# Kernel tuning notes

Hardware: AMD Instinct MI355X
Metric: run time of the kernel (lower is better)

## Reference

```python
import jax, jax.numpy as jnp
import numpy as np

B, CIN, T = 16, 80, 2048
C = 768          # channels
M = 512          # n_embeddings
D = 64           # z_dim
H = 256          # c_dim
N_MLP = 4        # hidden Linear(C, C) layers
LN_EPS = 1e-5
COMMIT = 0.25


def setup_inputs() -> dict:
    key = jax.random.key(0)
    ks = jax.random.split(key, 12)
    s = 0.02
    mels = jax.random.normal(ks[0], (B, CIN, T), dtype=jnp.float32)
    conv_w = jax.random.normal(ks[1], (C, CIN, 4), dtype=jnp.float32) * s  # [out, in, k]
    ln_gamma = jnp.ones((N_MLP + 1, C), dtype=jnp.float32)
    ln_beta = jnp.zeros((N_MLP + 1, C), dtype=jnp.float32)
    w_hidden = jax.random.normal(ks[2], (N_MLP, C, C), dtype=jnp.float32) * s  # [i, out, in]
    w_out = jax.random.normal(ks[3], (D, C), dtype=jnp.float32) * s
    embedding = jax.random.uniform(ks[4], (M, D), dtype=jnp.float32,
                                   minval=-1.0 / 512, maxval=1.0 / 512)
    w_ih = jax.random.normal(ks[5], (4 * H, D), dtype=jnp.float32) * s
    w_hh = jax.random.normal(ks[6], (4 * H, H), dtype=jnp.float32) * s
    b_ih = jnp.zeros((4 * H,), dtype=jnp.float32)
    b_hh = jnp.zeros((4 * H,), dtype=jnp.float32)
    return {"mels": mels, "conv_w": conv_w, "ln_gamma": ln_gamma, "ln_beta": ln_beta,
            "w_hidden": w_hidden, "w_out": w_out, "embedding": embedding,
            "w_ih": w_ih, "w_hh": w_hh, "b_ih": b_ih, "b_hh": b_hh}


def _layer_norm(x, g, b):
    mu = jnp.mean(x, axis=-1, keepdims=True)
    var = jnp.mean(jnp.square(x - mu), axis=-1, keepdims=True)
    return (x - mu) * jax.lax.rsqrt(var + LN_EPS) * g + b


def _lstm(x, w_ih, w_hh, b_ih, b_hh):
    # x: [B, T, D] -> outputs [B, T, H]; torch gate order i, f, g, o
    xg = jnp.einsum('btd,gd->btg', x, w_ih) + b_ih + b_hh  # precompute input gates

    def step(carry, xg_t):
        h, c = carry
        gates = xg_t + h @ w_hh.T
        i, f, g, o = jnp.split(gates, 4, axis=-1)
        c = jax.nn.sigmoid(f) * c + jax.nn.sigmoid(i) * jnp.tanh(g)
        h = jax.nn.sigmoid(o) * jnp.tanh(c)
        return (h, c), h

    h0 = jnp.zeros((x.shape[0], H), dtype=x.dtype)
    (_, _), hs = jax.lax.scan(step, (h0, h0), jnp.swapaxes(xg, 0, 1))
    return jnp.swapaxes(hs, 0, 1)


def reference(mels, conv_w, ln_gamma, ln_beta, w_hidden, w_out, embedding,
              w_ih, w_hh, b_ih, b_hh):
    # Conv1d(k=4, stride=2, pad=1, no bias): [B, CIN, T] -> [B, C, T//2]
    h = jax.lax.conv_general_dilated(
        mels, conv_w, window_strides=(2,), padding=[(1, 1)],
        dimension_numbers=('NCH', 'OIH', 'NCH'))
    h = jnp.swapaxes(h, 1, 2)  # [B, T', C]

    for i in range(N_MLP):
        h = jax.nn.relu(_layer_norm(h, ln_gamma[i], ln_beta[i]))
        h = h @ w_hidden[i].T
    h = jax.nn.relu(_layer_norm(h, ln_gamma[N_MLP], ln_beta[N_MLP]))
    z_beforeVQ = h @ w_out.T  # [B, T', D]

    # VQEmbeddingEMA forward (eval mode: no EMA buffer updates)
    x = z_beforeVQ
    x_flat = jax.lax.stop_gradient(x).reshape(-1, D)  # [N, D]
    dist = (jnp.sum(embedding ** 2, axis=1)[None, :]
            + jnp.sum(x_flat ** 2, axis=1, keepdims=True)
            - 2.0 * x_flat @ embedding.T)  # [N, M]
    indices = jnp.argmin(dist, axis=-1)
    quantized = embedding[indices].reshape(x.shape)
    loss = COMMIT * jnp.mean(jnp.square(x - jax.lax.stop_gradient(quantized)))
    quantized_st = x + jax.lax.stop_gradient(quantized - x)
    counts = jax.ops.segment_sum(jnp.ones_like(indices, dtype=jnp.float32),
                                 indices, num_segments=M)
    avg_probs = counts / x_flat.shape[0]
    perplexity = jnp.exp(-jnp.sum(avg_probs * jnp.log(avg_probs + 1e-10)))

    c = _lstm(quantized_st, w_ih, w_hh, b_ih, b_hh)  # [B, T', H]
    return quantized_st, c, z_beforeVQ, loss, perplexity
```

## Files before the change

kernel.cpp:

```cpp
#include <hip/hip_runtime.h>
#include <hip/hip_bf16.h>
#include <cstdint>

typedef _Float16 half2v __attribute__((ext_vector_type(2)));
typedef short bf16x8 __attribute__((ext_vector_type(8)));
typedef float f32x4v __attribute__((ext_vector_type(4)));

#define DI __device__ __forceinline__

DI half2v bch(float f)    { return __builtin_bit_cast(half2v, f); }
DI half2v bcu(unsigned u) { return __builtin_bit_cast(half2v, u); }

DI float fdot2f(half2v a, half2v b, float c) {
#if __has_builtin(__builtin_amdgcn_fdot2)
  return __builtin_amdgcn_fdot2(a, b, c, false);
#else
  return c + (float)a[0] * (float)b[0] + (float)a[1] * (float)b[1];
#endif
}

DI unsigned short bf16rne(float f) {
  unsigned u = __float_as_uint(f);
  unsigned r = (u + 0x7fffu + ((u >> 16) & 1u)) >> 16;
  return (unsigned short)r;
}
DI float bf16tof(unsigned short h) { return __uint_as_float(((unsigned)h) << 16); }

DI float blockReduceSum(float v, float* sbuf) {
  for (int off = 32; off; off >>= 1) v += __shfl_xor(v, off, 64);
  int wid = threadIdx.x >> 6;
  if ((threadIdx.x & 63) == 0) sbuf[wid] = v;
  __syncthreads();
  float r = sbuf[0] + sbuf[1] + sbuf[2] + sbuf[3];
  __syncthreads();
  return r;
}

__global__ __launch_bounds__(256) void prep_kernel(
    const float* __restrict__ conv_w, const float* __restrict__ w_hh,
    const float* __restrict__ w_ih, const float* __restrict__ b_ih,
    const float* __restrict__ b_hh, const float* __restrict__ emb,
    float* __restrict__ wT, _Float16* __restrict__ whhh,
    float* __restrict__ wihT, float* __restrict__ bias2,
    float* __restrict__ esq, int* __restrict__ counts)
{
  int idx = blockIdx.x * 256 + threadIdx.x;
  if (idx < 245760) {
    int c = idx % 768, rest = idx / 768;
    wT[idx] = conv_w[c * 320 + rest];
  }
  int i1 = idx - 245760;
  if (i1 >= 0 && i1 < 262144) whhh[i1] = (_Float16)w_hh[i1];
  int i2 = idx - (245760 + 262144);
  if (i2 >= 0 && i2 < 65536) {
    int d = i2 >> 10, grow = i2 & 1023;
    wihT[i2] = w_ih[grow * 64 + d];
  }
  int i3 = idx - (245760 + 262144 + 65536);
  if (i3 >= 0 && i3 < 1024) bias2[i3] = b_ih[i3] + b_hh[i3];
  int i4 = idx - (245760 + 262144 + 65536 + 1024);
  if (i4 >= 0 && i4 < 512) {
    float s = 0.f;
    for (int d = 0; d < 64; ++d) { float v = emb[i4 * 64 + d]; s += v * v; }
    esq[i4] = s;
  }
  int i5 = idx - (245760 + 262144 + 65536 + 1024 + 512);
  if (i5 >= 0 && i5 < 512) counts[i5] = 0;
}

__global__ __launch_bounds__(256) void wsplit_kernel(
    const float* __restrict__ w, unsigned short* __restrict__ whi,
    unsigned short* __restrict__ wlo)
{
  int idx = blockIdx.x * 256 + threadIdx.x;
  float v = w[idx];
  unsigned short h = bf16rne(v);
  whi[idx] = h;
  wlo[idx] = bf16rne(v - bf16tof(h));
}

__global__ __launch_bounds__(256) void conv_kernel(
    const float* __restrict__ mels, const float* __restrict__ wT,
    float* __restrict__ out)
{
  __shared__ float xs[80][68];
  const int bx = blockIdx.x;
  const int cblk = bx % 6;
  const int rb = bx / 6;
  const int b = rb >> 5;
  const int t0 = (rb & 31) << 5;
  const int tid = threadIdx.x;
  const int g0 = 2 * t0 - 1;
  for (int e = tid; e < 80 * 68; e += 256) {
    int ci = e / 68, ix = e % 68;
    int g = g0 + ix;
    float v = 0.f;
    if (ix < 67 && g >= 0 && g < 2048) v = mels[((size_t)b * 80 + ci) * 2048 + g];
    xs[ci][ix] = v;
  }
  __syncthreads();
  const int tc = tid & 31, tt = tid >> 5;
  const int c = cblk * 128 + tc * 4;
  float acc[4][4] = {};
  for (int ci = 0; ci < 80; ++ci) {
    float m[10];
#pragma unroll
    for (int r = 0; r < 10; ++r) m[r] = xs[ci][tt * 8 + r];
#pragma unroll
    for (int k = 0; k < 4; ++k) {
      float4 wv = *(const float4*)&wT[(size_t)(ci * 4 + k) * 768 + c];
#pragma unroll
      for (int i = 0; i < 4; ++i) {
        float mv = m[2 * i + k];
        acc[i][0] += mv * wv.x; acc[i][1] += mv * wv.y;
        acc[i][2] += mv * wv.z; acc[i][3] += mv * wv.w;
      }
    }
  }
#pragma unroll
  for (int i = 0; i < 4; ++i) {
    int tp = t0 + tt * 4 + i;
    float4 v = make_float4(acc[i][0], acc[i][1], acc[i][2], acc[i][3]);
    *(float4*)&out[((size_t)b * 1024 + tp) * 768 + c] = v;
  }
}

template<int MODE>
__global__ __launch_bounds__(256) void ln_relu_kernel(
    const float* __restrict__ in, float* __restrict__ outf,
    unsigned short* __restrict__ ohi, unsigned short* __restrict__ olo,
    const float* __restrict__ gamma, const float* __restrict__ beta)
{
  __shared__ float sbuf[4];
  const int row = blockIdx.x, tid = threadIdx.x;
  const float* p = in + (size_t)row * 768;
  float v0 = p[tid], v1 = p[tid + 256], v2 = p[tid + 512];
  float s = blockReduceSum(v0 + v1 + v2, sbuf);
  float mean = s * (1.f / 768.f);
  float d0 = v0 - mean, d1 = v1 - mean, d2 = v2 - mean;
  float sq = blockReduceSum(d0 * d0 + d1 * d1 + d2 * d2, sbuf);
  float rstd = rsqrtf(sq * (1.f / 768.f) + 1e-5f);
  float y0 = fmaxf(d0 * rstd * gamma[tid]       + beta[tid],       0.f);
  float y1 = fmaxf(d1 * rstd * gamma[tid + 256] + beta[tid + 256], 0.f);
  float y2 = fmaxf(d2 * rstd * gamma[tid + 512] + beta[tid + 512], 0.f);
  if (MODE == 0) {
    float* q = outf + (size_t)row * 768;
    q[tid] = y0; q[tid + 256] = y1; q[tid + 512] = y2;
  } else {
    unsigned short* qh = ohi + (size_t)row * 768;
    unsigned short* ql = olo + (size_t)row * 768;
    unsigned short h0 = bf16rne(y0), h1 = bf16rne(y1), h2 = bf16rne(y2);
    qh[tid] = h0; qh[tid + 256] = h1; qh[tid + 512] = h2;
    ql[tid]       = bf16rne(y0 - bf16tof(h0));
    ql[tid + 256] = bf16rne(y1 - bf16tof(h1));
    ql[tid + 512] = bf16rne(y2 - bf16tof(h2));
  }
}

__global__ __launch_bounds__(256) void mlp_gemm(
    const unsigned short* __restrict__ Ahi, const unsigned short* __restrict__ Alo,
    const unsigned short* __restrict__ Whi, const unsigned short* __restrict__ Wlo,
    float* __restrict__ C)
{
  __shared__ unsigned short As[128][40];
  __shared__ unsigned short Bs[128][40];
  const int tid = threadIdx.x;
  const int lane = tid & 63, wid = tid >> 6;
  const int wm = wid >> 1, wn = wid & 1;
  const int l15 = lane & 15, kg = lane >> 4;
  const size_t row0 = (size_t)blockIdx.y * 128;
  const int col0 = blockIdx.x * 128;
  f32x4v acc[4][4];
#pragma unroll
  for (int i = 0; i < 4; ++i)
#pragma unroll
    for (int j = 0; j < 4; ++j) acc[i][j] = (f32x4v){0.f, 0.f, 0.f, 0.f};
  for (int s = 0; s < 3; ++s) {
    const unsigned short* Ap = (s == 2) ? Alo : Ahi;
    const unsigned short* Wp = (s == 1) ? Wlo : Whi;
    for (int kt = 0; kt < 768; kt += 32) {
      __syncthreads();
#pragma unroll
      for (int it = 0; it < 2; ++it) {
        int sidx = tid + it * 256;
        int r = sidx >> 2, kc = (sidx & 3) << 3;
        uint4 va = *(const uint4*)&Ap[(row0 + r) * 768 + kt + kc];
        *(uint4*)&As[r][kc] = va;
        uint4 vb = *(const uint4*)&Wp[(size_t)(col0 + r) * 768 + kt + kc];
        *(uint4*)&Bs[r][kc] = vb;
      }
      __syncthreads();
      bf16x8 af[4], bfr[4];
#pragma unroll
      for (int mf = 0; mf < 4; ++mf)
        af[mf] = *(const bf16x8*)&As[wm * 64 + mf * 16 + l15][kg * 8];
#pragma unroll
      for (int nf = 0; nf < 4; ++nf)
        bfr[nf] = *(const bf16x8*)&Bs[wn * 64 + nf * 16 + l15][kg * 8];
#pragma unroll
      for (int mf = 0; mf < 4; ++mf)
#pragma unroll
        for (int nf = 0; nf < 4; ++nf)
          acc[mf][nf] = __builtin_amdgcn_mfma_f32_16x16x32_bf16(
              af[mf], bfr[nf], acc[mf][nf], 0, 0, 0);
    }
  }
#pragma unroll
  for (int mf = 0; mf < 4; ++mf)
#pragma unroll
    for (int nf = 0; nf < 4; ++nf)
#pragma unroll
      for (int r = 0; r < 4; ++r)
        C[(row0 + wm * 64 + mf * 16 + kg * 4 + r) * 768 +
          col0 + wn * 64 + nf * 16 + l15] = acc[mf][nf][r];
}

template<int BM, int BN, int BK, int TM, int TN>
__global__ __launch_bounds__(256) void gemm_nt(
    const float* __restrict__ A, const float* __restrict__ B,
    float* __restrict__ C, int M, int N, int K)
{
  constexpr int LDA = BM + 4, LDB = BN + 4;
  __shared__ float As[BK][LDA];
  __shared__ float Bs[BK][LDB];
  const int tid = threadIdx.x;
  const size_t row0 = (size_t)blockIdx.y * BM;
  const size_t col0 = (size_t)blockIdx.x * BN;
  const int tx = tid & 15, ty = tid >> 4;
  constexpr int GSM = BM * 4 / TM;
  constexpr int GSN = BN * 4 / TN;
  constexpr int F4R = BK / 4;
  constexpr int AIT = BM * BK / 4 / 256;
  constexpr int BIT = BN * BK / 4 / 256;
  static_assert(AIT * 256 * 4 == BM * BK, "A tile divisibility");
  static_assert(BIT * 256 * 4 == BN * BK, "B tile divisibility");
  float acc[TM][TN] = {};
  for (int kt = 0; kt < K; kt += BK) {
#pragma unroll
    for (int p = 0; p < AIT; ++p) {
      int item = tid + p * 256;
      int r = item / F4R, q = item % F4R;
      float4 v = *(const float4*)&A[(row0 + r) * K + kt + q * 4];
      As[q * 4 + 0][r] = v.x; As[q * 4 + 1][r] = v.y;
      As[q * 4 + 2][r] = v.z; As[q * 4 + 3][r] = v.w;
    }
#pragma unroll
    for (int p = 0; p < BIT; ++p) {
      int item = tid + p * 256;
      int r = item / F4R, q = item % F4R;
      float4 v = *(const float4*)&B[(col0 + r) * K + kt + q * 4];
      Bs[q * 4 + 0][r] = v.x; Bs[q * 4 + 1][r] = v.y;
      Bs[q * 4 + 2][r] = v.z; Bs[q * 4 + 3][r] = v.w;
    }
    __syncthreads();
#pragma unroll
    for (int k = 0; k < BK; ++k) {
      float a[TM], b[TN];
#pragma unroll
      for (int g = 0; g < TM / 4; ++g) {
        float4 v = *(const float4*)&As[k][ty * 4 + g * GSM];
        a[g * 4 + 0] = v.x; a[g * 4 + 1] = v.y; a[g * 4 + 2] = v.z; a[g * 4 + 3] = v.w;
      }
#pragma unroll
      for (int g = 0; g < TN / 4; ++g) {
        float4 v = *(const float4*)&Bs[k][tx * 4 + g * GSN];
        b[g * 4 + 0] = v.x; b[g * 4 + 1] = v.y; b[g * 4 + 2] = v.z; b[g * 4 + 3] = v.w;
      }
#pragma unroll
      for (int i = 0; i < TM; ++i)
#pragma unroll
        for (int j = 0; j < TN; ++j)
          acc[i][j] += a[i] * b[j];
    }
    __syncthreads();
  }
#pragma unroll
  for (int i = 0; i < TM; ++i) {
    size_t row = row0 + ty * 4 + (i >> 2) * GSM + (i & 3);
#pragma unroll
    for (int g = 0; g < TN / 4; ++g) {
      float4 v = make_float4(acc[i][g * 4 + 0], acc[i][g * 4 + 1],
                             acc[i][g * 4 + 2], acc[i][g * 4 + 3]);
      *(float4*)&C[row * N + col0 + tx * 4 + g * GSN] = v;
    }
  }
}

DI unsigned int ordbits(float f) {
  unsigned int u = __float_as_uint(f);
  return (u & 0x80000000u) ? ~u : (u | 0x80000000u);
}

__global__ __launch_bounds__(128) void vq_argmin_kernel(
    const float* __restrict__ dots, const float* __restrict__ esq,
    const float* __restrict__ emb, const float* __restrict__ z,
    float* __restrict__ quant, int* __restrict__ counts,
    float* __restrict__ lossrow)
{
  __shared__ unsigned long long sred[2];
  const int row = blockIdx.x, tid = threadIdx.x;
  float4 d4 = *(const float4*)&dots[(size_t)row * 512 + tid * 4];
  float4 e4 = *(const float4*)&esq[tid * 4];
  float dist[4] = { e4.x - 2.f * d4.x, e4.y - 2.f * d4.y,
                    e4.z - 2.f * d4.z, e4.w - 2.f * d4.w };
  unsigned long long best =
      ((unsigned long long)ordbits(dist[0]) << 32) | (unsigned)(tid * 4);
#pragma unroll
  for (int c2 = 1; c2 < 4; ++c2) {
    unsigned long long k =
        ((unsigned long long)ordbits(dist[c2]) << 32) | (unsigned)(tid * 4 + c2);
    best = (k < best) ? k : best;
  }
  for (int off = 32; off; off >>= 1) {
    unsigned long long o = __shfl_xor(best, off, 64);
    best = (o < best) ? o : best;
  }
  if ((tid & 63) == 0) sred[tid >> 6] = best;
  __syncthreads();
  unsigned long long fin = sred[0] < sred[1] ? sred[0] : sred[1];
  int bi = (int)(fin & 0xffffffffu);
  if (tid < 64) {
    float e = emb[(size_t)bi * 64 + tid];
    quant[(size_t)row * 64 + tid] = e;
    float df = z[(size_t)row * 64 + tid] - e;
    float s = df * df;
    for (int off = 32; off; off >>= 1) s += __shfl_xor(s, off, 64);
    if (tid == 0) {
      lossrow[row] = s;
      atomicAdd(&counts[bi], 1);
    }
  }
}

__global__ __launch_bounds__(256) void finalize_kernel(
    const float* __restrict__ lossrow, const int* __restrict__ counts,
    float* __restrict__ loss_out, float* __restrict__ perp_out)
{
  __shared__ float sbuf[4];
  const int tid = threadIdx.x;
  float s = 0.f;
  for (int i = tid; i < 16384; i += 256) s += lossrow[i];
  s = blockReduceSum(s, sbuf);
  float t = 0.f;
  for (int e = tid; e < 512; e += 256) {
    float p = (float)counts[e] * (1.f / 16384.f);
    t += p * logf(p + 1e-10f);
  }
  t = blockReduceSum(t, sbuf);
  if (tid == 0) {
    *loss_out = 0.25f * s / (16384.f * 64.f);
    *perp_out = expf(-t);
  }
}

__global__ __launch_bounds__(256) void xg_kernel(
    const float* __restrict__ q, const float* __restrict__ wihT,
    const float* __restrict__ bias2, float* __restrict__ xg3)
{
  __shared__ float qs[8][64];
  const int r0 = blockIdx.x * 8, tid = threadIdx.x;
  for (int e = tid; e < 512; e += 256)
    qs[e >> 6][e & 63] = q[(size_t)r0 * 64 + e];
  __syncthreads();
  float4 bias = *(const float4*)&bias2[tid * 4];
  float4 acc[8];
#pragma unroll
  for (int r = 0; r < 8; ++r) acc[r] = bias;
  for (int d = 0; d < 64; ++d) {
    float4 wv = *(const float4*)&wihT[d * 1024 + tid * 4];
#pragma unroll
    for (int r = 0; r < 8; ++r) {
      float qv = qs[r][d];
      acc[r].x += qv * wv.x; acc[r].y += qv * wv.y;
      acc[r].z += qv * wv.z; acc[r].w += qv * wv.w;
    }
  }
#pragma unroll
  for (int r = 0; r < 8; ++r)
    *(float4*)&xg3[(size_t)(r0 + r) * 1024 + tid * 4] = acc[r];
}

#define W24(M) M(0) M(1) M(2) M(3) M(4) M(5) M(6) M(7) M(8) M(9) M(10) M(11) \
               M(12) M(13) M(14) M(15) M(16) M(17) M(18) M(19) M(20) M(21) M(22) M(23)
#define DECLW(J) uint4 wa##J = pA[J]; uint4 wb##J = pB[J];
#define DOTR(J) { float4 h4 = hb4[J]; \
  a0 = fdot2f(bcu(wa##J.x), bch(h4.x), a0); b0 = fdot2f(bcu(wb##J.x), bch(h4.x), b0); \
  a1 = fdot2f(bcu(wa##J.y), bch(h4.y), a1); b1 = fdot2f(bcu(wb##J.y), bch(h4.y), b1); \
  a0 = fdot2f(bcu(wa##J.z), bch(h4.z), a0); b0 = fdot2f(bcu(wb##J.z), bch(h4.z), b0); \
  a1 = fdot2f(bcu(wa##J.w), bch(h4.w), a1); b1 = fdot2f(bcu(wb##J.w), bch(h4.w), b1); }

__global__
__attribute__((amdgpu_flat_work_group_size(512, 512), amdgpu_waves_per_eu(2, 2)))
void lstm_kernel(
    const float* __restrict__ xg3, const _Float16* __restrict__ whhh,
    float* __restrict__ cout)
{
  __shared__ unsigned wlds[1024 * 36];
  __shared__ __align__(16) _Float16 hb[256];
  __shared__ float gbuf[512];
  const int tid = threadIdx.x;
  const int b = blockIdx.x;
  const int jloc = tid & 255;
  const int half = tid >> 8;
  const int rA = half * 256 + jloc;
  const int rB = 512 + half * 256 + jloc;
  {
    const unsigned* wsrc = (const unsigned*)whhh;
    for (int idx = tid; idx < 1024 * 32; idx += 512) {
      int row = idx >> 5, kp = idx & 31;
      wlds[row * 36 + kp] = wsrc[row * 128 + 96 + kp];
    }
  }
  if (tid < 256) hb[tid] = (_Float16)0.f;
  const uint4* pA = (const uint4*)(whhh + (size_t)rA * 256);
  const uint4* pB = (const uint4*)(whhh + (size_t)rB * 256);
  W24(DECLW)
  const size_t bT = (size_t)b * 1024;
  const int rA36 = rA * 36, rB36 = rB * 36;
  float cst = 0.f;
  float xgA = xg3[bT * 1024 + rA];
  float xgB = xg3[bT * 1024 + rB];
  __syncthreads();
  for (int t = 0; t < 1024; ++t) {
    float nxA = 0.f, nxB = 0.f;
    if (t < 1023) {
      nxA = xg3[(bT + t + 1) * 1024 + rA];
      nxB = xg3[(bT + t + 1) * 1024 + rB];
    }
    float a0 = 0.f, a1 = 0.f, b0 = 0.f, b1 = 0.f;
    const float4* hb4 = (const float4*)hb;
    W24(DOTR)
#pragma unroll
    for (int j = 0; j < 8; ++j) {
      float4 h4 = hb4[24 + j];
      uint4 wa = *(const uint4*)&wlds[rA36 + 4 * j];
      uint4 wb = *(const uint4*)&wlds[rB36 + 4 * j];
      a0 = fdot2f(bcu(wa.x), bch(h4.x), a0); b0 = fdot2f(bcu(wb.x), bch(h4.x), b0);
      a1 = fdot2f(bcu(wa.y), bch(h4.y), a1); b1 = fdot2f(bcu(wb.y), bch(h4.y), b1);
      a0 = fdot2f(bcu(wa.z), bch(h4.z), a0); b0 = fdot2f(bcu(wb.z), bch(h4.z), b0);
      a1 = fdot2f(bcu(wa.w), bch(h4.w), a1); b1 = fdot2f(bcu(wb.w), bch(h4.w), b1);
    }
    float gA = a0 + a1 + xgA;
    float gB = b0 + b1 + xgB;
    if (half) { gbuf[jloc] = gA; gbuf[256 + jloc] = gB; }
    __syncthreads();
    if (!half) {
      float gf = gbuf[jloc], go = gbuf[256 + jloc];
      float si = 1.f / (1.f + __expf(-gA));
      float sf = 1.f / (1.f + __expf(-gf));
      float so = 1.f / (1.f + __expf(-go));
      float tg = 1.f - 2.f / (1.f + __expf(2.f * gB));
      cst = sf * cst + si * tg;
      float tc = 1.f - 2.f / (1.f + __expf(2.f * cst));
      float h = so * tc;
      cout[(bT + t) * 256 + jloc] = h;
      hb[jloc] = (_Float16)h;
    }
    __syncthreads();
    xgA = nxA; xgB = nxB;
  }
}

extern "C" void kernel_launch(void* const* d_in, const int* in_sizes, int n_in,
                              void* d_out, int out_size, void* d_ws, size_t ws_size,
                              hipStream_t stream)
{
  const float* mels   = (const float*)d_in[0];
  const float* conv_w = (const float*)d_in[1];
  const float* ln_g   = (const float*)d_in[2];
  const float* ln_b   = (const float*)d_in[3];
  const float* w_hid  = (const float*)d_in[4];
  const float* w_out  = (const float*)d_in[5];
  const float* emb    = (const float*)d_in[6];
  const float* w_ih   = (const float*)d_in[7];
  const float* w_hh   = (const float*)d_in[8];
  const float* b_ih   = (const float*)d_in[9];
  const float* b_hh   = (const float*)d_in[10];

  float* out = (float*)d_out;
  float* q_out   = out;
  float* c_out   = out + 1048576;
  float* z_out   = out + 5242880;
  float* loss_out = out + 6291456;
  float* perp_out = out + 6291457;

  char* ws = (char*)d_ws;
  float*  hA    = (float*)(ws + 0);
  float*  hB    = (float*)(ws + 50331648);
  unsigned short* Ahi = (unsigned short*)(ws + 50331648);
  unsigned short* Alo = (unsigned short*)(ws + 75497472);
  float*  dots  = (float*)(ws + 0);
  float*  xg3   = (float*)(ws + 50331648);
  char* wsw = ws + 117440512;
  float*    wT     = (float*)(wsw);
  _Float16* whhh   = (_Float16*)(wsw + 983040);
  float*    wihT   = (float*)(wsw + 1507328);
  float*    bias2  = (float*)(wsw + 1769472);
  float*    esq    = (float*)(wsw + 1773568);
  int*      counts = (int*)  (wsw + 1775616);
  float*    lossrow= (float*)(wsw + 1777664);
  unsigned short* Whi = (unsigned short*)((char*)d_out + 4194304);
  unsigned short* Wlo = Whi + 2359296;
  if (ws_size < 119283712u) return;

  prep_kernel<<<2248, 256, 0, stream>>>(conv_w, w_hh, w_ih, b_ih, b_hh, emb,
                                        wT, whhh, wihT, bias2, esq, counts);
  wsplit_kernel<<<9216, 256, 0, stream>>>(w_hid, Whi, Wlo);
  conv_kernel<<<3072, 256, 0, stream>>>(mels, wT, hA);
  for (int l = 0; l < 4; ++l) {
    ln_relu_kernel<1><<<16384, 256, 0, stream>>>(
        hA, nullptr, Ahi, Alo, ln_g + l * 768, ln_b + l * 768);
    mlp_gemm<<<dim3(6, 128), 256, 0, stream>>>(
        Ahi, Alo, Whi + (size_t)l * 589824, Wlo + (size_t)l * 589824, hA);
  }
  ln_relu_kernel<0><<<16384, 256, 0, stream>>>(
      hA, hB, nullptr, nullptr, ln_g + 4 * 768, ln_b + 4 * 768);
  gemm_nt<128, 64, 16, 8, 4><<<dim3(1, 128), 256, 0, stream>>>(
      hB, w_out, z_out, 16384, 64, 768);
  gemm_nt<128, 128, 16, 8, 8><<<dim3(4, 128), 256, 0, stream>>>(
      z_out, emb, dots, 16384, 512, 64);
  vq_argmin_kernel<<<16384, 128, 0, stream>>>(dots, esq, emb, z_out,
                                              q_out, counts, lossrow);
  finalize_kernel<<<1, 256, 0, stream>>>(lossrow, counts, loss_out, perp_out);
  xg_kernel<<<2048, 256, 0, stream>>>(q_out, wihT, bias2, xg3);
  lstm_kernel<<<16, 512, 0, stream>>>(xg3, whhh, c_out);
}
```

Before: 2.664 ms.

## Drop bf16x3 split for plain bf16 MLP GEMMs and fuse z/VQ tail

The hidden-layer GEMMs previously emulated fp32 with three bf16 MFMA passes (hi/lo splits). They now use a single bf16 pass, removing the lo arrays and two thirds of the MFMA work and operand traffic. The output projection, codebook distance GEMM and argmin are fused into one MFMA kernel that keeps z in shared memory, so the fp32 dots matrix is never written or re-read. The cost is lower precision: bf16 distances can flip the argmin for near-tied codes, and the fused tail launches only 128 blocks.

```diff
diff --git a/kernel.cpp b/kernel.cpp
--- a/kernel.cpp
+++ b/kernel.cpp
@@ -24,7 +24,11 @@
   unsigned r = (u + 0x7fffu + ((u >> 16) & 1u)) >> 16;
   return (unsigned short)r;
 }
-DI float bf16tof(unsigned short h) { return __uint_as_float(((unsigned)h) << 16); }
+
+DI unsigned int ordbits(float f) {
+  unsigned int u = __float_as_uint(f);
+  return (u & 0x80000000u) ? ~u : (u | 0x80000000u);
+}
 
 DI float blockReduceSum(float v, float* sbuf) {
   for (int off = 32; off; off >>= 1) v += __shfl_xor(v, off, 64);
@@ -68,15 +72,17 @@
   if (i5 >= 0 && i5 < 512) counts[i5] = 0;
 }
 
-__global__ __launch_bounds__(256) void wsplit_kernel(
-    const float* __restrict__ w, unsigned short* __restrict__ whi,
-    unsigned short* __restrict__ wlo)
+__global__ __launch_bounds__(256) void wcvt_kernel(
+    const float* __restrict__ w_hid, const float* __restrict__ w_out,
+    const float* __restrict__ emb, unsigned short* __restrict__ Whi,
+    unsigned short* __restrict__ Wzh, unsigned short* __restrict__ embh)
 {
   int idx = blockIdx.x * 256 + threadIdx.x;
-  float v = w[idx];
-  unsigned short h = bf16rne(v);
-  whi[idx] = h;
-  wlo[idx] = bf16rne(v - bf16tof(h));
+  if (idx < 2359296) Whi[idx] = bf16rne(w_hid[idx]);
+  int i1 = idx - 2359296;
+  if (i1 >= 0 && i1 < 49152) Wzh[i1] = bf16rne(w_out[i1]);
+  int i2 = idx - (2359296 + 49152);
+  if (i2 >= 0 && i2 < 32768) embh[i2] = bf16rne(emb[i2]);
 }
 
 __global__ __launch_bounds__(256) void conv_kernel(
@@ -125,10 +131,8 @@
   }
 }
 
-template<int MODE>
 __global__ __launch_bounds__(256) void ln_relu_kernel(
-    const float* __restrict__ in, float* __restrict__ outf,
-    unsigned short* __restrict__ ohi, unsigned short* __restrict__ olo,
+    const float* __restrict__ in, unsigned short* __restrict__ ohi,
     const float* __restrict__ gamma, const float* __restrict__ beta)
 {
   __shared__ float sbuf[4];
@@ -143,23 +147,12 @@
   float y0 = fmaxf(d0 * rstd * gamma[tid]       + beta[tid],       0.f);
   float y1 = fmaxf(d1 * rstd * gamma[tid + 256] + beta[tid + 256], 0.f);
   float y2 = fmaxf(d2 * rstd * gamma[tid + 512] + beta[tid + 512], 0.f);
-  if (MODE == 0) {
-    float* q = outf + (size_t)row * 768;
-    q[tid] = y0; q[tid + 256] = y1; q[tid + 512] = y2;
-  } else {
-    unsigned short* qh = ohi + (size_t)row * 768;
-    unsigned short* ql = olo + (size_t)row * 768;
-    unsigned short h0 = bf16rne(y0), h1 = bf16rne(y1), h2 = bf16rne(y2);
-    qh[tid] = h0; qh[tid + 256] = h1; qh[tid + 512] = h2;
-    ql[tid]       = bf16rne(y0 - bf16tof(h0));
-    ql[tid + 256] = bf16rne(y1 - bf16tof(h1));
-    ql[tid + 512] = bf16rne(y2 - bf16tof(h2));
-  }
+  unsigned short* qh = ohi + (size_t)row * 768;
+  qh[tid] = bf16rne(y0); qh[tid + 256] = bf16rne(y1); qh[tid + 512] = bf16rne(y2);
 }
 
 __global__ __launch_bounds__(256) void mlp_gemm(
-    const unsigned short* __restrict__ Ahi, const unsigned short* __restrict__ Alo,
-    const unsigned short* __restrict__ Whi, const unsigned short* __restrict__ Wlo,
+    const unsigned short* __restrict__ Ah, const unsigned short* __restrict__ Wh,
     float* __restrict__ C)
 {
   __shared__ unsigned short As[128][40];
@@ -175,35 +168,29 @@
   for (int i = 0; i < 4; ++i)
 #pragma unroll
     for (int j = 0; j < 4; ++j) acc[i][j] = (f32x4v){0.f, 0.f, 0.f, 0.f};
-  for (int s = 0; s < 3; ++s) {
-    const unsigned short* Ap = (s == 2) ? Alo : Ahi;
-    const unsigned short* Wp = (s == 1) ? Wlo : Whi;
-    for (int kt = 0; kt < 768; kt += 32) {
-      __syncthreads();
-#pragma unroll
-      for (int it = 0; it < 2; ++it) {
-        int sidx = tid + it * 256;
-        int r = sidx >> 2, kc = (sidx & 3) << 3;
-        uint4 va = *(const uint4*)&Ap[(row0 + r) * 768 + kt + kc];
-        *(uint4*)&As[r][kc] = va;
-        uint4 vb = *(const uint4*)&Wp[(size_t)(col0 + r) * 768 + kt + kc];
-        *(uint4*)&Bs[r][kc] = vb;
-      }
-      __syncthreads();
-      bf16x8 af[4], bfr[4];
-#pragma unroll
-      for (int mf = 0; mf < 4; ++mf)
-        af[mf] = *(const bf16x8*)&As[wm * 64 + mf * 16 + l15][kg * 8];
+  for (int kt = 0; kt < 768; kt += 32) {
+    __syncthreads();
+#pragma unroll
+    for (int it = 0; it < 2; ++it) {
+      int sidx = tid + it * 256;
+      int r = sidx >> 2, kc = (sidx & 3) << 3;
+      *(uint4*)&As[r][kc] = *(const uint4*)&Ah[(row0 + r) * 768 + kt + kc];
+      *(uint4*)&Bs[r][kc] = *(const uint4*)&Wh[(size_t)(col0 + r) * 768 + kt + kc];
+    }
+    __syncthreads();
+    bf16x8 af[4], bfr[4];
+#pragma unroll
+    for (int mf = 0; mf < 4; ++mf)
+      af[mf] = *(const bf16x8*)&As[wm * 64 + mf * 16 + l15][kg * 8];
+#pragma unroll
+    for (int nf = 0; nf < 4; ++nf)
+      bfr[nf] = *(const bf16x8*)&Bs[wn * 64 + nf * 16 + l15][kg * 8];
+#pragma unroll
+    for (int mf = 0; mf < 4; ++mf)
 #pragma unroll
       for (int nf = 0; nf < 4; ++nf)
-        bfr[nf] = *(const bf16x8*)&Bs[wn * 64 + nf * 16 + l15][kg * 8];
-#pragma unroll
-      for (int mf = 0; mf < 4; ++mf)
-#pragma unroll
-        for (int nf = 0; nf < 4; ++nf)
-          acc[mf][nf] = __builtin_amdgcn_mfma_f32_16x16x32_bf16(
-              af[mf], bfr[nf], acc[mf][nf], 0, 0, 0);
-    }
+        acc[mf][nf] = __builtin_amdgcn_mfma_f32_16x16x32_bf16(
+            af[mf], bfr[nf], acc[mf][nf], 0, 0, 0);
   }
 #pragma unroll
   for (int mf = 0; mf < 4; ++mf)
@@ -215,118 +202,153 @@
           col0 + wn * 64 + nf * 16 + l15] = acc[mf][nf][r];
 }
 
-template<int BM, int BN, int BK, int TM, int TN>
-__global__ __launch_bounds__(256) void gemm_nt(
-    const float* __restrict__ A, const float* __restrict__ B,
-    float* __restrict__ C, int M, int N, int K)
-{
-  constexpr int LDA = BM + 4, LDB = BN + 4;
-  __shared__ float As[BK][LDA];
-  __shared__ float Bs[BK][LDB];
-  const int tid = threadIdx.x;
-  const size_t row0 = (size_t)blockIdx.y * BM;
-  const size_t col0 = (size_t)blockIdx.x * BN;
-  const int tx = tid & 15, ty = tid >> 4;
-  constexpr int GSM = BM * 4 / TM;
-  constexpr int GSN = BN * 4 / TN;
-  constexpr int F4R = BK / 4;
-  constexpr int AIT = BM * BK / 4 / 256;
-  constexpr int BIT = BN * BK / 4 / 256;
-  static_assert(AIT * 256 * 4 == BM * BK, "A tile divisibility");
-  static_assert(BIT * 256 * 4 == BN * BK, "B tile divisibility");
-  float acc[TM][TN] = {};
-  for (int kt = 0; kt < K; kt += BK) {
-#pragma unroll
-    for (int p = 0; p < AIT; ++p) {
-      int item = tid + p * 256;
-      int r = item / F4R, q = item % F4R;
-      float4 v = *(const float4*)&A[(row0 + r) * K + kt + q * 4];
-      As[q * 4 + 0][r] = v.x; As[q * 4 + 1][r] = v.y;
-      As[q * 4 + 2][r] = v.z; As[q * 4 + 3][r] = v.w;
-    }
-#pragma unroll
-    for (int p = 0; p < BIT; ++p) {
-      int item = tid + p * 256;
-      int r = item / F4R, q = item % F4R;
-      float4 v = *(const float4*)&B[(col0 + r) * K + kt + q * 4];
-      Bs[q * 4 + 0][r] = v.x; Bs[q * 4 + 1][r] = v.y;
-      Bs[q * 4 + 2][r] = v.z; Bs[q * 4 + 3][r] = v.w;
-    }
-    __syncthreads();
-#pragma unroll
-    for (int k = 0; k < BK; ++k) {
-      float a[TM], b[TN];
-#pragma unroll
-      for (int g = 0; g < TM / 4; ++g) {
-        float4 v = *(const float4*)&As[k][ty * 4 + g * GSM];
-        a[g * 4 + 0] = v.x; a[g * 4 + 1] = v.y; a[g * 4 + 2] = v.z; a[g * 4 + 3] = v.w;
-      }
-#pragma unroll
-      for (int g = 0; g < TN / 4; ++g) {
-        float4 v = *(const float4*)&Bs[k][tx * 4 + g * GSN];
-        b[g * 4 + 0] = v.x; b[g * 4 + 1] = v.y; b[g * 4 + 2] = v.z; b[g * 4 + 3] = v.w;
-      }
-#pragma unroll
-      for (int i = 0; i < TM; ++i)
-#pragma unroll
-        for (int j = 0; j < TN; ++j)
-          acc[i][j] += a[i] * b[j];
-    }
-    __syncthreads();
-  }
-#pragma unroll
-  for (int i = 0; i < TM; ++i) {
-    size_t row = row0 + ty * 4 + (i >> 2) * GSM + (i & 3);
-#pragma unroll
-    for (int g = 0; g < TN / 4; ++g) {
-      float4 v = make_float4(acc[i][g * 4 + 0], acc[i][g * 4 + 1],
-                             acc[i][g * 4 + 2], acc[i][g * 4 + 3]);
-      *(float4*)&C[row * N + col0 + tx * 4 + g * GSN] = v;
-    }
-  }
-}
-
-DI unsigned int ordbits(float f) {
-  unsigned int u = __float_as_uint(f);
-  return (u & 0x80000000u) ? ~u : (u | 0x80000000u);
-}
-
-__global__ __launch_bounds__(128) void vq_argmin_kernel(
-    const float* __restrict__ dots, const float* __restrict__ esq,
-    const float* __restrict__ emb, const float* __restrict__ z,
+__global__ __launch_bounds__(256) void ztail_kernel(
+    const unsigned short* __restrict__ A4h, const unsigned short* __restrict__ Wzh,
+    const unsigned short* __restrict__ embh, const float* __restrict__ esq,
+    const float* __restrict__ emb, float* __restrict__ z_out,
     float* __restrict__ quant, int* __restrict__ counts,
     float* __restrict__ lossrow)
 {
-  __shared__ unsigned long long sred[2];
-  const int row = blockIdx.x, tid = threadIdx.x;
-  float4 d4 = *(const float4*)&dots[(size_t)row * 512 + tid * 4];
-  float4 e4 = *(const float4*)&esq[tid * 4];
-  float dist[4] = { e4.x - 2.f * d4.x, e4.y - 2.f * d4.y,
-                    e4.z - 2.f * d4.z, e4.w - 2.f * d4.w };
-  unsigned long long best =
-      ((unsigned long long)ordbits(dist[0]) << 32) | (unsigned)(tid * 4);
-#pragma unroll
-  for (int c2 = 1; c2 < 4; ++c2) {
-    unsigned long long k =
-        ((unsigned long long)ordbits(dist[c2]) << 32) | (unsigned)(tid * 4 + c2);
-    best = (k < best) ? k : best;
-  }
-  for (int off = 32; off; off >>= 1) {
-    unsigned long long o = __shfl_xor(best, off, 64);
-    best = (o < best) ? o : best;
-  }
-  if ((tid & 63) == 0) sred[tid >> 6] = best;
-  __syncthreads();
-  unsigned long long fin = sred[0] < sred[1] ? sred[0] : sred[1];
-  int bi = (int)(fin & 0xffffffffu);
-  if (tid < 64) {
-    float e = emb[(size_t)bi * 64 + tid];
-    quant[(size_t)row * 64 + tid] = e;
-    float df = z[(size_t)row * 64 + tid] - e;
-    float s = df * df;
-    for (int off = 32; off; off >>= 1) s += __shfl_xor(s, off, 64);
-    if (tid == 0) {
-      lossrow[row] = s;
+  __shared__ unsigned short As[128][40];
+  __shared__ unsigned short Ws[64][40];
+  __shared__ unsigned short zh[128][88];
+  __shared__ float zf[128][68];
+  __shared__ unsigned short embs[128][88];
+  __shared__ unsigned long long best2[2][128];
+  __shared__ float esqs[512];
+  const int tid = threadIdx.x;
+  const int lane = tid & 63, wid = tid >> 6;
+  const int wm = wid >> 1, wn = wid & 1;
+  const int l15 = lane & 15, kg = lane >> 4;
+  const size_t row0 = (size_t)blockIdx.x * 128;
+  for (int i = tid; i < 512; i += 256) esqs[i] = esq[i];
+  f32x4v zacc[4][2];
+#pragma unroll
+  for (int i = 0; i < 4; ++i)
+#pragma unroll
+    for (int j = 0; j < 2; ++j) zacc[i][j] = (f32x4v){0.f, 0.f, 0.f, 0.f};
+  for (int kt = 0; kt < 768; kt += 32) {
+    __syncthreads();
+#pragma unroll
+    for (int it = 0; it < 2; ++it) {
+      int sidx = tid + it * 256;
+      int r = sidx >> 2, kc = (sidx & 3) << 3;
+      *(uint4*)&As[r][kc] = *(const uint4*)&A4h[(row0 + r) * 768 + kt + kc];
+    }
+    { int r = tid >> 2, kc = (tid & 3) << 3;
+      *(uint4*)&Ws[r][kc] = *(const uint4*)&Wzh[r * 768 + kt + kc]; }
+    __syncthreads();
+    bf16x8 af[4], bfr[2];
+#pragma unroll
+    for (int mf = 0; mf < 4; ++mf)
+      af[mf] = *(const bf16x8*)&As[wm * 64 + mf * 16 + l15][kg * 8];
+#pragma unroll
+    for (int nf = 0; nf < 2; ++nf)
+      bfr[nf] = *(const bf16x8*)&Ws[wn * 32 + nf * 16 + l15][kg * 8];
+#pragma unroll
+    for (int mf = 0; mf < 4; ++mf)
+#pragma unroll
+      for (int nf = 0; nf < 2; ++nf)
+        zacc[mf][nf] = __builtin_amdgcn_mfma_f32_16x16x32_bf16(
+            af[mf], bfr[nf], zacc[mf][nf], 0, 0, 0);
+  }
+#pragma unroll
+  for (int mf = 0; mf < 4; ++mf)
+#pragma unroll
+    for (int nf = 0; nf < 2; ++nf)
+#pragma unroll
+      for (int r = 0; r < 4; ++r) {
+        float v = zacc[mf][nf][r];
+        int rr = wm * 64 + mf * 16 + kg * 4 + r;
+        int cc = wn * 32 + nf * 16 + l15;
+        zf[rr][cc] = v;
+        zh[rr][cc] = bf16rne(v);
+        z_out[(row0 + rr) * 64 + cc] = v;
+      }
+  if (tid < 128) { best2[0][tid] = ~0ull; best2[1][tid] = ~0ull; }
+  __syncthreads();
+  for (int c0 = 0; c0 < 512; c0 += 128) {
+    __syncthreads();
+#pragma unroll
+    for (int ii = 0; ii < 4; ++ii) {
+      int s = tid * 4 + ii;
+      int code = s >> 3, k = (s & 7) << 3;
+      *(uint4*)&embs[code][k] = *(const uint4*)&embh[(size_t)(c0 + code) * 64 + k];
+    }
+    __syncthreads();
+    bf16x8 af2[4][2], bf2[4][2];
+#pragma unroll
+    for (int mf = 0; mf < 4; ++mf)
+#pragma unroll
+      for (int kk = 0; kk < 2; ++kk)
+        af2[mf][kk] = *(const bf16x8*)&zh[wm * 64 + mf * 16 + l15][kk * 32 + kg * 8];
+#pragma unroll
+    for (int nf = 0; nf < 4; ++nf)
+#pragma unroll
+      for (int kk = 0; kk < 2; ++kk)
+        bf2[nf][kk] = *(const bf16x8*)&embs[wn * 64 + nf * 16 + l15][kk * 32 + kg * 8];
+#pragma unroll
+    for (int mf = 0; mf < 4; ++mf) {
+      f32x4v dacc[4];
+#pragma unroll
+      for (int nf = 0; nf < 4; ++nf) {
+        dacc[nf] = (f32x4v){0.f, 0.f, 0.f, 0.f};
+        dacc[nf] = __builtin_amdgcn_mfma_f32_16x16x32_bf16(
+            af2[mf][0], bf2[nf][0], dacc[nf], 0, 0, 0);
+        dacc[nf] = __builtin_amdgcn_mfma_f32_16x16x32_bf16(
+            af2[mf][1], bf2[nf][1], dacc[nf], 0, 0, 0);
+      }
+      unsigned long long rb0 = ~0ull, rb1 = ~0ull, rb2 = ~0ull, rb3 = ~0ull;
+#pragma unroll
+      for (int nf = 0; nf < 4; ++nf) {
+        int code = c0 + wn * 64 + nf * 16 + l15;
+        float ev = esqs[code];
+        unsigned long long k0 = ((unsigned long long)ordbits(ev - 2.f * dacc[nf][0]) << 32) | (unsigned)code;
+        unsigned long long k1 = ((unsigned long long)ordbits(ev - 2.f * dacc[nf][1]) << 32) | (unsigned)code;
+        unsigned long long k2 = ((unsigned long long)ordbits(ev - 2.f * dacc[nf][2]) << 32) | (unsigned)code;
+        unsigned long long k3 = ((unsigned long long)ordbits(ev - 2.f * dacc[nf][3]) << 32) | (unsigned)code;
+        rb0 = k0 < rb0 ? k0 : rb0;  rb1 = k1 < rb1 ? k1 : rb1;
+        rb2 = k2 < rb2 ? k2 : rb2;  rb3 = k3 < rb3 ? k3 : rb3;
+      }
+#pragma unroll
+      for (int m = 1; m < 16; m <<= 1) {
+        unsigned long long o;
+        o = __shfl_xor(rb0, m, 64); rb0 = o < rb0 ? o : rb0;
+        o = __shfl_xor(rb1, m, 64); rb1 = o < rb1 ? o : rb1;
+        o = __shfl_xor(rb2, m, 64); rb2 = o < rb2 ? o : rb2;
+        o = __shfl_xor(rb3, m, 64); rb3 = o < rb3 ? o : rb3;
+      }
+      if (l15 == 0) {
+        int rbase = wm * 64 + mf * 16 + kg * 4;
+        unsigned long long c;
+        c = best2[wn][rbase + 0]; best2[wn][rbase + 0] = rb0 < c ? rb0 : c;
+        c = best2[wn][rbase + 1]; best2[wn][rbase + 1] = rb1 < c ? rb1 : c;
+        c = best2[wn][rbase + 2]; best2[wn][rbase + 2] = rb2 < c ? rb2 : c;
+        c = best2[wn][rbase + 3]; best2[wn][rbase + 3] = rb3 < c ? rb3 : c;
+      }
+    }
+  }
+  __syncthreads();
+  if (tid < 128) {
+    unsigned long long a = best2[0][tid], b = best2[1][tid];
+    best2[0][tid] = b < a ? b : a;
+  }
+  __syncthreads();
+  {
+    int rr = tid >> 1, hf = tid & 1;
+    int bi = (int)(best2[0][rr] & 0xffffffffu);
+    float ls = 0.f;
+#pragma unroll
+    for (int dd = 0; dd < 32; ++dd) {
+      int d = hf * 32 + dd;
+      float e = emb[(size_t)bi * 64 + d];
+      quant[(row0 + rr) * 64 + d] = e;
+      float df = zf[rr][d] - e;
+      ls += df * df;
+    }
+    ls += __shfl_xor(ls, 1, 64);
+    if (hf == 0) {
+      lossrow[row0 + rr] = ls;
       atomicAdd(&counts[bi], 1);
     }
   }
@@ -486,10 +508,7 @@
 
   char* ws = (char*)d_ws;
   float*  hA    = (float*)(ws + 0);
-  float*  hB    = (float*)(ws + 50331648);
   unsigned short* Ahi = (unsigned short*)(ws + 50331648);
-  unsigned short* Alo = (unsigned short*)(ws + 75497472);
-  float*  dots  = (float*)(ws + 0);
   float*  xg3   = (float*)(ws + 50331648);
   char* wsw = ws + 117440512;
   float*    wT     = (float*)(wsw);
@@ -499,28 +518,23 @@
   float*    esq    = (float*)(wsw + 1773568);
   int*      counts = (int*)  (wsw + 1775616);
   float*    lossrow= (float*)(wsw + 1777664);
-  unsigned short* Whi = (unsigned short*)((char*)d_out + 4194304);
-  unsigned short* Wlo = Whi + 2359296;
+  unsigned short* Whi  = (unsigned short*)((char*)d_out + 4194304);
+  unsigned short* Wzh  = (unsigned short*)((char*)d_out + 4194304 + 4718592);
+  unsigned short* embh = (unsigned short*)((char*)d_out + 4194304 + 4718592 + 98304);
   if (ws_size < 119283712u) return;
 
   prep_kernel<<<2248, 256, 0, stream>>>(conv_w, w_hh, w_ih, b_ih, b_hh, emb,
                                         wT, whhh, wihT, bias2, esq, counts);
-  wsplit_kernel<<<9216, 256, 0, stream>>>(w_hid, Whi, Wlo);
+  wcvt_kernel<<<9536, 256, 0, stream>>>(w_hid, w_out, emb, Whi, Wzh, embh);
   conv_kernel<<<3072, 256, 0, stream>>>(mels, wT, hA);
   for (int l = 0; l < 4; ++l) {
-    ln_relu_kernel<1><<<16384, 256, 0, stream>>>(
-        hA, nullptr, Ahi, Alo, ln_g + l * 768, ln_b + l * 768);
+    ln_relu_kernel<<<16384, 256, 0, stream>>>(hA, Ahi, ln_g + l * 768, ln_b + l * 768);
     mlp_gemm<<<dim3(6, 128), 256, 0, stream>>>(
-        Ahi, Alo, Whi + (size_t)l * 589824, Wlo + (size_t)l * 589824, hA);
-  }
-  ln_relu_kernel<0><<<16384, 256, 0, stream>>>(
-      hA, hB, nullptr, nullptr, ln_g + 4 * 768, ln_b + 4 * 768);
-  gemm_nt<128, 64, 16, 8, 4><<<dim3(1, 128), 256, 0, stream>>>(
-      hB, w_out, z_out, 16384, 64, 768);
-  gemm_nt<128, 128, 16, 8, 8><<<dim3(4, 128), 256, 0, stream>>>(
-      z_out, emb, dots, 16384, 512, 64);
-  vq_argmin_kernel<<<16384, 128, 0, stream>>>(dots, esq, emb, z_out,
-                                              q_out, counts, lossrow);
+        Ahi, Whi + (size_t)l * 589824, hA);
+  }
+  ln_relu_kernel<<<16384, 256, 0, stream>>>(hA, Ahi, ln_g + 4 * 768, ln_b + 4 * 768);
+  ztail_kernel<<<128, 256, 0, stream>>>(Ahi, Wzh, embh, esq, emb,
+                                        z_out, q_out, counts, lossrow);
   finalize_kernel<<<1, 256, 0, stream>>>(lossrow, counts, loss_out, perp_out);
   xg_kernel<<<2048, 256, 0, stream>>>(q_out, wihT, bias2, xg3);
   lstm_kernel<<<16, 512, 0, stream>>>(xg3, whhh, c_out);
```

New measurement: 2.250 ms. 15.5% less time.
